# Kernel tuning notes

Hardware: AMD Instinct MI355X
Metric: run time of the kernel (lower is better)

Reference implementation:

```python
import jax, jax.numpy as jnp
import numpy as np

OUTPUT_DIM = 2
HIDDEN_DIM = 512
NUM_MODES = 6
PRED_LEN = 60
BATCH = 8192


def setup_inputs() -> dict:
    key = jax.random.key(0)
    ks = jax.random.split(key, 12)
    H, D, M = HIDDEN_DIM, OUTPUT_DIM, NUM_MODES
    s = 1.0 / np.sqrt(H)  # PyTorch default uniform(-1/sqrt(H), 1/sqrt(H))
    u = lambda k, shape: jax.random.uniform(k, shape, jnp.float32, -s, s)
    return {
        "social_features": jax.random.normal(ks[0], (BATCH, H), jnp.float32),
        "hidden": jax.random.normal(ks[1], (1, BATCH, H), jnp.float32),
        "cell": jax.random.normal(ks[2], (1, BATCH, H), jnp.float32),
        "w_ih": u(ks[3], (4 * H, D + H)),   # LSTM input->gates (i,f,g,o)
        "w_hh": u(ks[4], (4 * H, H)),       # LSTM hidden->gates
        "b_ih": u(ks[5], (4 * H,)),
        "b_hh": u(ks[6], (4 * H,)),
        "w_out": u(ks[7], (D * M, H)),      # output_layer
        "b_out": u(ks[8], (D * M,)),
        "w_mode": u(ks[9], (M, H)),         # mode_prob_layer
        "b_mode": u(ks[10], (M,)),
        "pred_len": PRED_LEN,
    }


def _decode(social_features, hidden, cell, w_ih, w_hh, b_ih, b_hh,
            w_out, b_out, w_mode, b_mode, pred_len):
    B = social_features.shape[0]
    H, D, M = HIDDEN_DIM, OUTPUT_DIM, NUM_MODES
    h0 = hidden[0]  # num_layers == 1
    c0 = cell[0]
    x0 = jnp.zeros((B, D), social_features.dtype)
    bias = b_ih + b_hh

    def step(carry, _):
        x, h, c = carry
        inp = jnp.concatenate([x, social_features], axis=-1)  # [B, D+H]
        gates = inp @ w_ih.T + h @ w_hh.T + bias              # [B, 4H]
        i, f, g, o = jnp.split(gates, 4, axis=-1)             # PyTorch gate order
        i = jax.nn.sigmoid(i)
        f = jax.nn.sigmoid(f)
        g = jnp.tanh(g)
        o = jax.nn.sigmoid(o)
        c_new = f * c + i * g
        h_new = o * jnp.tanh(c_new)
        pred = (h_new @ w_out.T + b_out).reshape(B, M, D)     # [B, M, D]
        mode_prob = jax.nn.softmax(h_new @ w_mode.T + b_mode, axis=-1)  # [B, M]
        x_next = pred[:, 0, :]
        return (x_next, h_new, c_new), (pred, mode_prob)

    _, (preds, probs) = jax.lax.scan(step, (x0, h0, c0), None, length=pred_len)
    # scan stacks on leading time axis -> move to batch-first
    predictions = jnp.transpose(preds, (1, 0, 2, 3))  # [B, T, M, D]
    mode_probs = jnp.transpose(probs, (1, 0, 2))      # [B, T, M]
    return predictions, mode_probs


def reference(social_features, hidden, cell, w_ih, w_hh, b_ih, b_hh,
              w_out, b_out, w_mode, b_mode, pred_len):
    return _decode(social_features, hidden, cell, w_ih, w_hh, b_ih, b_hh,
                   w_out, b_out, w_mode, b_mode, pred_len)
```

## Files before the change

kernel.cpp:

```cpp
#include <hip/hip_runtime.h>

#define H 512
#define BATCHN 8192
#define STEPS 60
#define NWGS 256

#define WEFF_OFF   0u
#define WPLAIN_OFF 2097152u
#define WIHS_OFF   4194304u
#define WSM_OFF    6291456u
#define BSM_OFF    6324224u
#define BX1_OFF    6324352u
#define BX0_OFF    6332544u
#define BAR_OFF    6340736u
#define XCDT_OFF   6340864u
#define FLAGS_OFF  6341888u
#define HB0_OFF    8388608u
#define HB1_OFF    16777216u
#define CPACK_OFF  25165824u
#define SPACK_OFF  41943040u

typedef short s16x8 __attribute__((ext_vector_type(8)));
typedef float f32x4 __attribute__((ext_vector_type(4)));
typedef unsigned int u32x2 __attribute__((ext_vector_type(2)));
typedef unsigned int u32x4 __attribute__((ext_vector_type(4)));

__device__ inline unsigned f2bf(float f) {
  unsigned u = __builtin_bit_cast(unsigned, f);
  return (u + 0x7fffu + ((u >> 16) & 1u)) >> 16;
}
__device__ inline float bf2f(unsigned s) {
  return __builtin_bit_cast(float, s << 16);
}
__device__ inline float sigm(float x) {
  float e = __builtin_amdgcn_exp2f(-1.442695041f * x);
  return __builtin_amdgcn_rcpf(1.0f + e);
}
__device__ inline float tanh_(float x) {
  float e = __builtin_amdgcn_exp2f(2.885390082f * x);
  return 1.0f - 2.0f * __builtin_amdgcn_rcpf(1.0f + e);
}
__device__ inline f32x4 mfma16(s16x8 a, s16x8 b, f32x4 c) {
  return __builtin_amdgcn_mfma_f32_16x16x32_bf16(a, b, c, 0, 0, 0);
}
__device__ inline int haddr(int b, int k) {
  return b * 1024 + ((k * 2) ^ ((b & 7) << 4));
}

__device__ inline void vm_drain() {
  asm volatile("s_waitcnt vmcnt(0)" ::: "memory");
  __builtin_amdgcn_sched_barrier(0);
}

__device__ inline void stage_issue(const unsigned short* h_in, int b0, int p, int tid,
                                   bool fast, u32x4 sreg[4]) {
  const char* pb = (const char*)h_in + (size_t)(b0 + p * 32 + (tid >> 4)) * 1024 +
                   (tid & 15) * 64;
  if (fast) {
    asm volatile("global_load_dwordx4 %0, %1, off sc0" : "=v"(sreg[0]) : "v"(pb));
    asm volatile("global_load_dwordx4 %0, %1, off offset:16 sc0" : "=v"(sreg[1]) : "v"(pb));
    asm volatile("global_load_dwordx4 %0, %1, off offset:32 sc0" : "=v"(sreg[2]) : "v"(pb));
    asm volatile("global_load_dwordx4 %0, %1, off offset:48 sc0" : "=v"(sreg[3]) : "v"(pb));
  } else {
    asm volatile("global_load_dwordx4 %0, %1, off sc0 sc1" : "=v"(sreg[0]) : "v"(pb));
    asm volatile("global_load_dwordx4 %0, %1, off offset:16 sc0 sc1" : "=v"(sreg[1]) : "v"(pb));
    asm volatile("global_load_dwordx4 %0, %1, off offset:32 sc0 sc1" : "=v"(sreg[2]) : "v"(pb));
    asm volatile("global_load_dwordx4 %0, %1, off offset:48 sc0 sc1" : "=v"(sreg[3]) : "v"(pb));
  }
}
__device__ inline void stage_write(unsigned short* buf, int tid, const u32x4 sreg[4]) {
  int row = tid >> 4;
  char* b = (char*)buf + row * 1024;
  int off = (tid & 15) * 64;
  #pragma unroll
  for (int i = 0; i < 4; ++i)
    *(u32x4*)(b + ((off + i * 16) ^ ((row & 7) << 4))) = sreg[i];
}

__device__ inline void global_barrier_once(unsigned* bar) {
  __syncthreads();
  if (threadIdx.x == 0) {
    unsigned a = __hip_atomic_fetch_add(bar, 1u, __ATOMIC_ACQ_REL, __HIP_MEMORY_SCOPE_AGENT);
    if (a == NWGS - 1) {
      __hip_atomic_store(bar + 16, 1u, __ATOMIC_RELEASE, __HIP_MEMORY_SCOPE_AGENT);
    } else {
      #pragma unroll 1
      while (__hip_atomic_load(bar + 16, __ATOMIC_ACQUIRE, __HIP_MEMORY_SCOPE_AGENT) == 0u)
        __builtin_amdgcn_s_sleep(2);
    }
  }
  __syncthreads();
}

__global__ void pack_kernel(const float* __restrict__ w_ih, const float* __restrict__ w_hh,
                            const float* __restrict__ w_out, const float* __restrict__ b_out,
                            const float* __restrict__ w_mode, const float* __restrict__ b_mode,
                            unsigned char* __restrict__ ws) {
  unsigned idx = blockIdx.x * 256 + threadIdx.x;
  if (idx < 2097152u) {
    unsigned j = idx & 1048575u;
    bool eff = idx < 1048576u;
    unsigned e = j & 7u, lane = (j >> 3) & 63u, kb = (j >> 9) & 15u, T = j >> 13;
    unsigned i = lane & 15u;
    unsigned hcol = T * 4u + (i >> 2), gate = i & 3u;
    unsigned n = gate * 512u + hcol;
    unsigned k = kb * 32u + (lane >> 4) * 8u + e;
    float v = w_hh[(size_t)n * 512u + k];
    if (eff) v += w_ih[(size_t)n * 514u] * w_out[k] + w_ih[(size_t)n * 514u + 1u] * w_out[512u + k];
    ((unsigned short*)(ws + (eff ? WEFF_OFF : WPLAIN_OFF)))[j] = (unsigned short)f2bf(v);
  } else if (idx < 3145728u) {
    unsigned j = idx - 2097152u;
    unsigned e = j & 7u, lane = (j >> 3) & 63u, kb = (j >> 9) & 15u, nb = j >> 13;
    unsigned n = nb * 16u + (lane & 15u), k = kb * 32u + (lane >> 4) * 8u + e;
    ((unsigned short*)(ws + WIHS_OFF))[j] = (unsigned short)f2bf(w_ih[(size_t)n * 514u + 2u + k]);
  } else if (idx < 3162112u) {
    unsigned j = idx - 3145728u;
    unsigned e = j & 7u, lane = (j >> 3) & 63u, kb = (j >> 9) & 15u, nb = j >> 13;
    unsigned o = nb * 16u + (lane & 15u), k = kb * 32u + (lane >> 4) * 8u + e;
    float v = 0.0f;
    if (o < 12u) v = w_out[o * 512u + k];
    else if (o < 18u) v = w_mode[(o - 12u) * 512u + k];
    ((unsigned short*)(ws + WSM_OFF))[j] = (unsigned short)f2bf(v);
  } else if (idx < 3162144u) {
    unsigned o = idx - 3162112u;
    float v = 0.0f;
    if (o < 12u) v = b_out[o];
    else if (o < 18u) v = b_mode[o - 12u];
    ((float*)(ws + BSM_OFF))[o] = v;
  } else if (idx < 3164192u) {
    unsigned m = idx - 3162144u;
    unsigned T = m >> 4, i = m & 15u;
    unsigned hcol = T * 4u + (i >> 2), gate = i & 3u;
    unsigned n = gate * 512u + hcol;
    ((float*)(ws + BX1_OFF))[m] = w_ih[(size_t)n * 514u] * b_out[0] + w_ih[(size_t)n * 514u + 1u] * b_out[1];
  } else if (idx < 3166240u) {
    ((float*)(ws + BX0_OFF))[idx - 3164192u] = 0.0f;
  } else if (idx < 3166272u) {
    ((unsigned*)(ws + BAR_OFF))[idx - 3166240u] = 0u;
  } else if (idx < 3166528u) {
    ((unsigned*)(ws + XCDT_OFF))[idx - 3166272u] = 0xFFFFFFFFu;
  } else if (idx < 3168576u) {
    ((unsigned*)(ws + FLAGS_OFF))[idx - 3166528u] = 0u;
  }
}

__global__ __launch_bounds__(512, 2) void prep_kernel(
    const float* __restrict__ social, const float* __restrict__ hidden,
    const float* __restrict__ cell, const float* __restrict__ b_ih,
    const float* __restrict__ b_hh, unsigned char* __restrict__ ws) {
  const int tid = threadIdx.x;
  const int wid = tid >> 6;
  const int lane = tid & 63;
  const int q = lane >> 4;
  const int r = lane & 15;
  const int wg = blockIdx.x;
  const int gb0 = wg * 32;

  const s16x8* wihs_w = (const s16x8*)(ws + WIHS_OFF) + (size_t)wid * 4096 + lane;
  unsigned short* spack = (unsigned short*)(ws + SPACK_OFF);
  unsigned short* hb0 = (unsigned short*)(ws + HB0_OFF);
  float* cpackp = (float*)(ws + CPACK_OFF);

  __shared__ unsigned short h_lds[32 * H];

  s16x8 wbuf[4][4];
  #pragma unroll
  for (int d = 0; d < 4; ++d)
    #pragma unroll
    for (int g = 0; g < 4; ++g)
      wbuf[d][g] = wihs_w[g * 32768 + d * 64];

  #pragma unroll
  for (int i = 0; i < 8; ++i) {
    int rr = i * 4 + (tid >> 7);
    int kk = (tid & 127) * 4;
    f32x4 v = *(const f32x4*)(social + (size_t)(gb0 + rr) * H + kk);
    u32x2 p;
    p[0] = f2bf(v[0]) | (f2bf(v[1]) << 16);
    p[1] = f2bf(v[2]) | (f2bf(v[3]) << 16);
    *(u32x2*)((char*)h_lds + haddr(rr, kk)) = p;
  }
  __syncthreads();

  #pragma unroll
  for (int jb = 0; jb < 4; ++jb) {
    f32x4 acc[4][2];
    #pragma unroll
    for (int g = 0; g < 4; ++g) {
      int n0 = g * 512 + wid * 64 + jb * 16 + q * 4;
      f32x4 bi = *(const f32x4*)(b_ih + n0);
      f32x4 bh = *(const f32x4*)(b_hh + n0);
      f32x4 bias = bi + bh;
      acc[g][0] = bias; acc[g][1] = bias;
    }
    #pragma unroll
    for (int kb = 0; kb < 16; ++kb) {
      const int F = jb * 16 + kb;
      const int slot = F & 3;
      s16x8 bfrag[2];
      #pragma unroll
      for (int bb = 0; bb < 2; ++bb)
        bfrag[bb] = *(const s16x8*)((char*)h_lds + haddr(bb * 16 + r, kb * 32 + q * 8));
      s16x8 af[4];
      #pragma unroll
      for (int g = 0; g < 4; ++g) af[g] = wbuf[slot][g];
      {
        const int Fn = (F + 4) & 63;
        const int jn = Fn >> 4, kn = Fn & 15;
        #pragma unroll
        for (int g = 0; g < 4; ++g)
          wbuf[slot][g] = wihs_w[g * 32768 + jn * 1024 + kn * 64];
      }
      #pragma unroll
      for (int g = 0; g < 4; ++g) {
        acc[g][0] = mfma16(af[g], bfrag[0], acc[g][0]);
        acc[g][1] = mfma16(af[g], bfrag[1], acc[g][1]);
      }
    }
    #pragma unroll
    for (int bb = 0; bb < 2; ++bb) {
      unsigned wrd[8];
      #pragma unroll
      for (int j = 0; j < 8; ++j) {
        int e = j >> 1, gp = (j & 1) * 2;
        wrd[j] = f2bf(acc[gp][bb][e]) | (f2bf(acc[gp + 1][bb][e]) << 16);
      }
      int T = wid * 16 + jb * 4 + q;
      int b = gb0 + bb * 16 + r;
      char* dst = (char*)spack + ((size_t)T * 8192 + b) * 32;
      u32x4 w0; w0[0] = wrd[0]; w0[1] = wrd[1]; w0[2] = wrd[2]; w0[3] = wrd[3];
      u32x4 w1; w1[0] = wrd[4]; w1[1] = wrd[5]; w1[2] = wrd[6]; w1[3] = wrd[7];
      *(u32x4*)dst = w0;
      *(u32x4*)(dst + 16) = w1;
    }
  }

  {
    const float* hsrc = hidden + (size_t)gb0 * H;
    unsigned short* hdst = hb0 + (size_t)gb0 * H;
    int base = tid * 32;
    #pragma unroll
    for (int v8 = 0; v8 < 4; ++v8) {
      f32x4 x0 = *(const f32x4*)(hsrc + base + v8 * 8);
      f32x4 x1 = *(const f32x4*)(hsrc + base + v8 * 8 + 4);
      u32x4 pk;
      pk[0] = f2bf(x0[0]) | (f2bf(x0[1]) << 16);
      pk[1] = f2bf(x0[2]) | (f2bf(x0[3]) << 16);
      pk[2] = f2bf(x1[0]) | (f2bf(x1[1]) << 16);
      pk[3] = f2bf(x1[2]) | (f2bf(x1[3]) << 16);
      *(u32x4*)(hdst + base + v8 * 8) = pk;
    }
  }

  for (int j = 0; j < 32; ++j) {
    int flat = tid * 32 + j;
    int b = gb0 + (flat >> 9);
    int hcol = flat & 511;
    float v = cell[(size_t)b * 512 + hcol];
    int jg2 = hcol >> 6, w2 = (hcol >> 3) & 7, Tl = (hcol >> 2) & 1, q2 = hcol & 3;
    int bg2 = b >> 8, ib2 = (b >> 4) & 15, r2 = b & 15;
    int wg2 = jg2 * 32 + bg2;
    cpackp[(((size_t)(wg2 * 8 + w2) * 16 + ib2) * 2 + Tl) * 64 + q2 * 16 + r2] = v;
  }
}

__global__ __attribute__((amdgpu_flat_work_group_size(512, 512), amdgpu_waves_per_eu(2, 2)))
void coop_kernel(
    const s16x8* __restrict__ weff, const s16x8* __restrict__ wplain,
    const float* __restrict__ bx, const unsigned short* __restrict__ spack,
    const s16x8* __restrict__ wsm, const float* __restrict__ bsm,
    unsigned short* __restrict__ hb0, unsigned short* __restrict__ hb1,
    float* __restrict__ cpack, float* __restrict__ out,
    unsigned* __restrict__ flags, unsigned* __restrict__ xcdt,
    unsigned* __restrict__ bar) {
  const int tid = threadIdx.x;
  const int wid = tid >> 6;
  const int lane = tid & 63;
  const int q = lane >> 4;
  const int r = lane & 15;
  const int wg = blockIdx.x;
  const int jg = wg >> 5;
  const int bg = wg & 31;
  const int b0 = bg * 256;
  const size_t MODE_BASE = (size_t)BATCHN * 720;

  __shared__ s16x8 wsm_lds[2048];
  __shared__ unsigned short hinA[32 * 512];
  __shared__ unsigned short hinB[32 * 512];
  __shared__ unsigned short hout_lds[256 * 64];
  __shared__ float mode_lds[8][16][8];
  __shared__ int fastf_lds;

  unsigned xcd;
  asm volatile("s_getreg_b32 %0, hwreg(20, 0, 32)" : "=s"(xcd));
  if (tid == 0)
    __hip_atomic_store(&xcdt[wg], xcd & 0xFu, __ATOMIC_RELEASE, __HIP_MEMORY_SCOPE_AGENT);

  s16x8 A0[16], A1[16];
  {
    const s16x8* ab = wplain + (size_t)((jg * 16 + wid * 2) * 16) * 64 + lane;
    #pragma unroll
    for (int kb = 0; kb < 16; ++kb) {
      asm volatile("global_load_dwordx4 %0, %1, off" : "=v"(A0[kb]) : "v"(ab + kb * 64));
      asm volatile("global_load_dwordx4 %0, %1, off" : "=v"(A1[kb]) : "v"(ab + kb * 64 + 1024));
    }
  }
  vm_drain();

  float* cb = cpack + (size_t)(wg * 8 + wid) * 2048 + lane;

  #pragma unroll
  for (int i = 0; i < 4; ++i) wsm_lds[i * 512 + tid] = wsm[i * 512 + tid];

  const char* sp0 = (const char*)spack + ((size_t)(jg * 16 + wid * 2 + 0) * 8192) * 32 + q * 8;
  const char* sp1 = (const char*)spack + ((size_t)(jg * 16 + wid * 2 + 1) * 8192) * 32 + q * 8;

  global_barrier_once(bar);
  if (tid == 0) {
    unsigned mine = xcd & 0xFu;
    bool same = true;
    for (int j = 0; j < 8; ++j) {
      unsigned v = __hip_atomic_load(&xcdt[bg + 32 * j], __ATOMIC_ACQUIRE, __HIP_MEMORY_SCOPE_AGENT);
      same = same && (v == mine);
    }
    fastf_lds = same ? 1 : 0;
  }
  __syncthreads();
  const bool fast = (fastf_lds != 0);

  #pragma unroll 1
  for (int s = 0; s < STEPS; ++s) {
    const unsigned short* h_in = (s & 1) ? hb1 : hb0;
    unsigned short* h_out = (s & 1) ? hb0 : hb1;
    f32x4 bxv0 = *(const f32x4*)(bx + (jg * 16 + wid * 2 + 0) * 16 + q * 4);
    f32x4 bxv1 = *(const f32x4*)(bx + (jg * 16 + wid * 2 + 1) * 16 + q * 4);
    if (s == 0) {
      f32x4 z = {0.f, 0.f, 0.f, 0.f};
      bxv0 = z; bxv1 = z;
    }

    u32x4 sreg[4];
    stage_issue(h_in, b0, 0, tid, fast, sreg);
    vm_drain();
    stage_write(hinA, tid, sreg);
    stage_issue(h_in, b0, 1, tid, fast, sreg);
    u32x2 sv0 = *(const u32x2*)(sp0 + (size_t)(b0 + r) * 32);
    u32x2 sv1 = *(const u32x2*)(sp1 + (size_t)(b0 + r) * 32);
    float cvn0 = cb[0], cvn1 = cb[64];
    __syncthreads();

    #pragma unroll
    for (int rr = 0; rr < 8; ++rr) {
      if (rr < 7) {
        unsigned short* wb = ((rr + 1) & 1) ? hinB : hinA;
        vm_drain();
        stage_write(wb, tid, sreg);
        if (rr < 6) stage_issue(h_in, b0, rr + 2, tid, fast, sreg);
      }
      const unsigned short* hbuf = (rr & 1) ? hinB : hinA;
      const bool dop = (wid == rr) && (s > 0);
      #pragma unroll
      for (int ib2 = 0; ib2 < 2; ++ib2) {
        const int bt = rr * 2 + ib2;
        const int b = b0 + bt * 16 + r;
        u32x2 cs0 = sv0, cs1 = sv1;
        float cva0 = cvn0, cva1 = cvn1;
        if (bt < 15) {
          sv0 = *(const u32x2*)(sp0 + (size_t)(b + 16) * 32);
          sv1 = *(const u32x2*)(sp1 + (size_t)(b + 16) * 32);
          cvn0 = cb[(bt + 1) * 128];
          cvn1 = cb[(bt + 1) * 128 + 64];
        }
        f32x4 acc0, acc1;
        acc0[0] = bf2f(cs0[0] & 0xffffu) + bxv0[0];
        acc0[1] = bf2f(cs0[0] >> 16)     + bxv0[1];
        acc0[2] = bf2f(cs0[1] & 0xffffu) + bxv0[2];
        acc0[3] = bf2f(cs0[1] >> 16)     + bxv0[3];
        acc1[0] = bf2f(cs1[0] & 0xffffu) + bxv1[0];
        acc1[1] = bf2f(cs1[0] >> 16)     + bxv1[1];
        acc1[2] = bf2f(cs1[1] & 0xffffu) + bxv1[2];
        acc1[3] = bf2f(cs1[1] >> 16)     + bxv1[3];
        #pragma unroll
        for (int kb = 0; kb < 16; ++kb) {
          s16x8 bfrag = *(const s16x8*)((const char*)hbuf + (ib2 * 16 + r) * 1024 +
                          ((kb * 64 + q * 16) ^ ((r & 7) << 4)));
          acc0 = mfma16(A0[kb], bfrag, acc0);
          acc1 = mfma16(A1[kb], bfrag, acc1);
        }
        #pragma unroll
        for (int Tl = 0; Tl < 2; ++Tl) {
          f32x4 ac = Tl ? acc1 : acc0;
          float cold = Tl ? cva1 : cva0;
          float iv = sigm(ac[0]), fv = sigm(ac[1]), gv = tanh_(ac[2]), ov = sigm(ac[3]);
          float cn = fv * cold + iv * gv;
          cb[bt * 128 + Tl * 64] = cn;
          float hn = ov * tanh_(cn);
          int col = wid * 8 + Tl * 4 + q;
          int row = bt * 16 + r;
          *(unsigned short*)((char*)hout_lds + row * 128 + ((col * 2) ^ ((r & 7) << 4))) =
              (unsigned short)f2bf(hn);
        }
        if (dop) {
          const int tprev = s - 1;
          f32x4 p0 = *(const f32x4*)(bsm + q * 4);
          f32x4 p1 = *(const f32x4*)(bsm + 16 + q * 4);
          #pragma unroll
          for (int kb = 0; kb < 16; ++kb) {
            s16x8 bfrag = *(const s16x8*)((const char*)hbuf + (ib2 * 16 + r) * 1024 +
                            ((kb * 64 + q * 16) ^ ((r & 7) << 4)));
            p0 = mfma16(wsm_lds[kb * 64 + lane], bfrag, p0);
            p1 = mfma16(wsm_lds[(16 + kb) * 64 + lane], bfrag, p1);
          }
          if (q < 3) *(f32x4*)(out + ((size_t)b * 60 + tprev) * 12 + q * 4) = p0;
          if (q == 3) *(f32x4*)(&mode_lds[wid][r][0]) = p0;
          if (q == 0) { mode_lds[wid][r][4] = p1[0]; mode_lds[wid][r][5] = p1[1]; }
          if (q == 1) {
            float v0 = mode_lds[wid][r][0], v1 = mode_lds[wid][r][1], v2 = mode_lds[wid][r][2];
            float v3 = mode_lds[wid][r][3], v4 = mode_lds[wid][r][4], v5 = mode_lds[wid][r][5];
            float mx = fmaxf(fmaxf(fmaxf(v0, v1), fmaxf(v2, v3)), fmaxf(v4, v5));
            float e0 = __builtin_amdgcn_exp2f(1.442695041f * (v0 - mx));
            float e1 = __builtin_amdgcn_exp2f(1.442695041f * (v1 - mx));
            float e2 = __builtin_amdgcn_exp2f(1.442695041f * (v2 - mx));
            float e3 = __builtin_amdgcn_exp2f(1.442695041f * (v3 - mx));
            float e4 = __builtin_amdgcn_exp2f(1.442695041f * (v4 - mx));
            float e5 = __builtin_amdgcn_exp2f(1.442695041f * (v5 - mx));
            float su = e0 + e1 + e2 + e3 + e4 + e5;
            float inv = __builtin_amdgcn_rcpf(su);
            float* mo = out + MODE_BASE + (size_t)b * 360 + tprev * 6;
            mo[0] = e0 * inv; mo[1] = e1 * inv; mo[2] = e2 * inv;
            mo[3] = e3 * inv; mo[4] = e4 * inv; mo[5] = e5 * inv;
          }
        }
      }
      __syncthreads();
    }
    {
      int row = tid >> 1;
      int off0 = (tid & 1) * 64;
      u32x4 v0 = *(const u32x4*)((const char*)hout_lds + row * 128 + ((off0 +  0) ^ ((row & 7) << 4)));
      u32x4 v1 = *(const u32x4*)((const char*)hout_lds + row * 128 + ((off0 + 16) ^ ((row & 7) << 4)));
      u32x4 v2 = *(const u32x4*)((const char*)hout_lds + row * 128 + ((off0 + 32) ^ ((row & 7) << 4)));
      u32x4 v3 = *(const u32x4*)((const char*)hout_lds + row * 128 + ((off0 + 48) ^ ((row & 7) << 4)));
      char* dst = (char*)h_out + (size_t)(b0 + row) * 1024 + jg * 128 + off0;
      if (fast) {
        asm volatile(
            "global_store_dwordx4 %0, %1, off\n\t"
            "global_store_dwordx4 %0, %2, off offset:16\n\t"
            "global_store_dwordx4 %0, %3, off offset:32\n\t"
            "global_store_dwordx4 %0, %4, off offset:48"
            :: "v"(dst), "v"(v0), "v"(v1), "v"(v2), "v"(v3) : "memory");
      } else {
        asm volatile(
            "global_store_dwordx4 %0, %1, off sc0 sc1\n\t"
            "global_store_dwordx4 %0, %2, off offset:16 sc0 sc1\n\t"
            "global_store_dwordx4 %0, %3, off offset:32 sc0 sc1\n\t"
            "global_store_dwordx4 %0, %4, off offset:48 sc0 sc1"
            :: "v"(dst), "v"(v0), "v"(v1), "v"(v2), "v"(v3) : "memory");
      }
      asm volatile("s_waitcnt vmcnt(0)" ::: "memory");
    }
    if (s < STEPS - 1) {
      __syncthreads();
      if (tid == 0) {
        unsigned* f = &flags[bg * 64 + s];
        __hip_atomic_fetch_add(f, 1u, __ATOMIC_RELAXED, __HIP_MEMORY_SCOPE_AGENT);
        unsigned v;
        #pragma unroll 1
        do {
          v = __hip_atomic_load(f, __ATOMIC_RELAXED, __HIP_MEMORY_SCOPE_AGENT);
          if (v < 8u) __builtin_amdgcn_s_sleep(1);
        } while (v < 8u);
      }
      __syncthreads();
    }
    if (s == 0) {
      const s16x8* ab = weff + (size_t)((jg * 16 + wid * 2) * 16) * 64 + lane;
      #pragma unroll
      for (int kb = 0; kb < 16; ++kb) {
        asm volatile("global_load_dwordx4 %0, %1, off" : "=v"(A0[kb]) : "v"(ab + kb * 64));
        asm volatile("global_load_dwordx4 %0, %1, off" : "=v"(A1[kb]) : "v"(ab + kb * 64 + 1024));
      }
      vm_drain();
    }
  }
}

__global__ __launch_bounds__(256) void projf_kernel(
    const unsigned short* __restrict__ h_in, const s16x8* __restrict__ wsm,
    const float* __restrict__ bsm, float* __restrict__ out) {
  const int tid = threadIdx.x;
  const int wid = tid >> 6;
  const int lane = tid & 63;
  const int q = lane >> 4;
  const int r = lane & 15;
  const int wg = blockIdx.x;
  const int b0 = wg * 32;
  const int bt = wid & 1, T = wid >> 1;
  const size_t MODE_BASE = (size_t)BATCHN * 720;
  __shared__ float mbuf[32][8];

  u32x4 hf[16];
  const char* hbase = (const char*)h_in + (size_t)(b0 + bt * 16 + r) * 1024 + q * 16;
  #pragma unroll
  for (int g = 0; g < 16; ++g) {
    asm volatile("global_load_dwordx4 %0, %1, off sc0 sc1"
                 : "=v"(hf[g]) : "v"(hbase + g * 64));
  }
  asm volatile("s_waitcnt vmcnt(0)" ::: "memory");
  __builtin_amdgcn_sched_barrier(0);

  f32x4 pacc = *(const f32x4*)(bsm + T * 16 + q * 4);
  #pragma unroll
  for (int kb = 0; kb < 16; ++kb) {
    s16x8 bfrag = __builtin_bit_cast(s16x8, hf[kb]);
    s16x8 af = wsm[(T * 16 + kb) * 64 + lane];
    pacc = mfma16(af, bfrag, pacc);
  }
  int b = b0 + bt * 16 + r;
  if (T == 0) {
    if (q < 3) *(f32x4*)(out + ((size_t)b * 60 + 59) * 12 + q * 4) = pacc;
    if (q == 3) *(f32x4*)(&mbuf[bt * 16 + r][0]) = pacc;
  } else {
    if (q == 0) { mbuf[bt * 16 + r][4] = pacc[0]; mbuf[bt * 16 + r][5] = pacc[1]; }
  }
  __syncthreads();
  if (tid < 32) {
    float v0 = mbuf[tid][0], v1 = mbuf[tid][1], v2 = mbuf[tid][2];
    float v3 = mbuf[tid][3], v4 = mbuf[tid][4], v5 = mbuf[tid][5];
    float mx = fmaxf(fmaxf(fmaxf(v0, v1), fmaxf(v2, v3)), fmaxf(v4, v5));
    float e0 = __builtin_amdgcn_exp2f(1.442695041f * (v0 - mx));
    float e1 = __builtin_amdgcn_exp2f(1.442695041f * (v1 - mx));
    float e2 = __builtin_amdgcn_exp2f(1.442695041f * (v2 - mx));
    float e3 = __builtin_amdgcn_exp2f(1.442695041f * (v3 - mx));
    float e4 = __builtin_amdgcn_exp2f(1.442695041f * (v4 - mx));
    float e5 = __builtin_amdgcn_exp2f(1.442695041f * (v5 - mx));
    float s = e0 + e1 + e2 + e3 + e4 + e5;
    float inv = __builtin_amdgcn_rcpf(s);
    float* mo = out + MODE_BASE + (size_t)(b0 + tid) * 360 + 59 * 6;
    mo[0] = e0 * inv; mo[1] = e1 * inv; mo[2] = e2 * inv;
    mo[3] = e3 * inv; mo[4] = e4 * inv; mo[5] = e5 * inv;
  }
}

extern "C" void kernel_launch(void* const* d_in, const int* in_sizes, int n_in,
                              void* d_out, int out_size, void* d_ws, size_t ws_size,
                              hipStream_t stream) {
  const float* social = (const float*)d_in[0];
  const float* hidden = (const float*)d_in[1];
  const float* cell   = (const float*)d_in[2];
  const float* w_ih   = (const float*)d_in[3];
  const float* w_hh   = (const float*)d_in[4];
  const float* b_ih   = (const float*)d_in[5];
  const float* b_hh   = (const float*)d_in[6];
  const float* w_out  = (const float*)d_in[7];
  const float* b_out  = (const float*)d_in[8];
  const float* w_mode = (const float*)d_in[9];
  const float* b_mode = (const float*)d_in[10];
  unsigned char* ws = (unsigned char*)d_ws;
  float* out = (float*)d_out;

  hipLaunchKernelGGL(pack_kernel, dim3((3168576u + 255u) / 256u), dim3(256), 0, stream,
                     w_ih, w_hh, w_out, b_out, w_mode, b_mode, ws);
  hipLaunchKernelGGL(prep_kernel, dim3(256), dim3(512), 0, stream,
                     social, hidden, cell, b_ih, b_hh, ws);

  const s16x8* weff   = (const s16x8*)(ws + WEFF_OFF);
  const s16x8* wplain = (const s16x8*)(ws + WPLAIN_OFF);
  const s16x8* wsm    = (const s16x8*)(ws + WSM_OFF);
  const float* bsm    = (const float*)(ws + BSM_OFF);
  const float* bx1    = (const float*)(ws + BX1_OFF);
  const unsigned short* spack = (const unsigned short*)(ws + SPACK_OFF);
  unsigned short* hb0p = (unsigned short*)(ws + HB0_OFF);
  unsigned short* hb1p = (unsigned short*)(ws + HB1_OFF);
  float* cpackc = (float*)(ws + CPACK_OFF);
  unsigned* flagsp = (unsigned*)(ws + FLAGS_OFF);
  unsigned* xcdtp = (unsigned*)(ws + XCDT_OFF);
  unsigned* barp = (unsigned*)(ws + BAR_OFF);

  void* args[] = {(void*)&weff, (void*)&wplain, (void*)&bx1, (void*)&spack,
                  (void*)&wsm, (void*)&bsm, (void*)&hb0p, (void*)&hb1p,
                  (void*)&cpackc, (void*)&out, (void*)&flagsp, (void*)&xcdtp,
                  (void*)&barp};
  hipLaunchCooperativeKernel((const void*)coop_kernel, dim3(NWGS), dim3(512),
                             args, 0, stream);

  hipLaunchKernelGGL(projf_kernel, dim3(256), dim3(256), 0, stream,
                     hb0p, wsm, bsm, out);
}
```

Measured before the change: 4.103 ms.

## Restructure per-round load pipeline with counted vmcnt waits and LDS-cached biases

Reworks the inner round loop of the persistent LSTM kernel so the h-tile staging write and the next-next issue happen after the MFMA compute instead of before it. Cell-state and social-precompute loads for a whole round are issued ahead through inline asm. Full vmcnt(0) drains become partial waits so loads overlap compute. Bias vectors (bx, bsm) are cached in LDS, and stores go through inline asm so they do not disturb the vmcnt accounting. Correctness depends on the hand-counted vmcnt values matching the actual order of outstanding loads and stores.

```diff
diff --git a/kernel.cpp b/kernel.cpp
--- a/kernel.cpp
+++ b/kernel.cpp
@@ -46,28 +46,14 @@
 __device__ inline int haddr(int b, int k) {
   return b * 1024 + ((k * 2) ^ ((b & 7) << 4));
 }
-
 __device__ inline void vm_drain() {
   asm volatile("s_waitcnt vmcnt(0)" ::: "memory");
   __builtin_amdgcn_sched_barrier(0);
 }
-
-__device__ inline void stage_issue(const unsigned short* h_in, int b0, int p, int tid,
-                                   bool fast, u32x4 sreg[4]) {
-  const char* pb = (const char*)h_in + (size_t)(b0 + p * 32 + (tid >> 4)) * 1024 +
-                   (tid & 15) * 64;
-  if (fast) {
-    asm volatile("global_load_dwordx4 %0, %1, off sc0" : "=v"(sreg[0]) : "v"(pb));
-    asm volatile("global_load_dwordx4 %0, %1, off offset:16 sc0" : "=v"(sreg[1]) : "v"(pb));
-    asm volatile("global_load_dwordx4 %0, %1, off offset:32 sc0" : "=v"(sreg[2]) : "v"(pb));
-    asm volatile("global_load_dwordx4 %0, %1, off offset:48 sc0" : "=v"(sreg[3]) : "v"(pb));
-  } else {
-    asm volatile("global_load_dwordx4 %0, %1, off sc0 sc1" : "=v"(sreg[0]) : "v"(pb));
-    asm volatile("global_load_dwordx4 %0, %1, off offset:16 sc0 sc1" : "=v"(sreg[1]) : "v"(pb));
-    asm volatile("global_load_dwordx4 %0, %1, off offset:32 sc0 sc1" : "=v"(sreg[2]) : "v"(pb));
-    asm volatile("global_load_dwordx4 %0, %1, off offset:48 sc0 sc1" : "=v"(sreg[3]) : "v"(pb));
-  }
-}
+#define WAITV(n) do { \
+  asm volatile("s_waitcnt vmcnt(" #n ")" ::: "memory"); \
+  __builtin_amdgcn_sched_barrier(0); } while (0)
+
 __device__ inline void stage_write(unsigned short* buf, int tid, const u32x4 sreg[4]) {
   int row = tid >> 4;
   char* b = (char*)buf + row * 1024;
@@ -289,6 +275,8 @@
   __shared__ unsigned short hinB[32 * 512];
   __shared__ unsigned short hout_lds[256 * 64];
   __shared__ float mode_lds[8][16][8];
+  __shared__ float bx_lds[256];
+  __shared__ float bsm_lds[32];
   __shared__ int fastf_lds;
 
   unsigned xcd;
@@ -308,12 +296,13 @@
   vm_drain();
 
   float* cb = cpack + (size_t)(wg * 8 + wid) * 2048 + lane;
+  const char* sp0b = (const char*)spack + ((size_t)(jg * 16 + wid * 2 + 0) * 8192 + (b0 + r)) * 32 + q * 8;
+  const char* sp1b = (const char*)spack + ((size_t)(jg * 16 + wid * 2 + 1) * 8192 + (b0 + r)) * 32 + q * 8;
 
   #pragma unroll
   for (int i = 0; i < 4; ++i) wsm_lds[i * 512 + tid] = wsm[i * 512 + tid];
-
-  const char* sp0 = (const char*)spack + ((size_t)(jg * 16 + wid * 2 + 0) * 8192) * 32 + q * 8;
-  const char* sp1 = (const char*)spack + ((size_t)(jg * 16 + wid * 2 + 1) * 8192) * 32 + q * 8;
+  if (tid < 256) bx_lds[tid] = bx[jg * 256 + tid];
+  if (tid < 32) bsm_lds[tid] = bsm[tid];
 
   global_barrier_once(bar);
   if (tid == 0) {
@@ -328,58 +317,82 @@
   __syncthreads();
   const bool fast = (fastf_lds != 0);
 
+  u32x4 sreg[4];
+  u32x2 sv_e0, sv_e1, sv_o0, sv_o1;
+  float cv_e0, cv_e1, cv_o0, cv_o1;
+
+#define ISSUE_H(p) do { \
+    const char* pb_ = (const char*)h_in + (size_t)(b0 + (p) * 32 + (tid >> 4)) * 1024 + (tid & 15) * 64; \
+    if (fast) { \
+      asm volatile("global_load_dwordx4 %0, %1, off sc0" : "=v"(sreg[0]) : "v"(pb_)); \
+      asm volatile("global_load_dwordx4 %0, %1, off offset:16 sc0" : "=v"(sreg[1]) : "v"(pb_)); \
+      asm volatile("global_load_dwordx4 %0, %1, off offset:32 sc0" : "=v"(sreg[2]) : "v"(pb_)); \
+      asm volatile("global_load_dwordx4 %0, %1, off offset:48 sc0" : "=v"(sreg[3]) : "v"(pb_)); \
+    } else { \
+      asm volatile("global_load_dwordx4 %0, %1, off sc0 sc1" : "=v"(sreg[0]) : "v"(pb_)); \
+      asm volatile("global_load_dwordx4 %0, %1, off offset:16 sc0 sc1" : "=v"(sreg[1]) : "v"(pb_)); \
+      asm volatile("global_load_dwordx4 %0, %1, off offset:32 sc0 sc1" : "=v"(sreg[2]) : "v"(pb_)); \
+      asm volatile("global_load_dwordx4 %0, %1, off offset:48 sc0 sc1" : "=v"(sreg[3]) : "v"(pb_)); \
+    } } while (0)
+
+#define ISSUE_SC(p) do { \
+    asm volatile("global_load_dwordx2 %0, %1, off" : "=v"(sv_e0) : "v"(sp0b + (p) * 1024)); \
+    asm volatile("global_load_dwordx2 %0, %1, off" : "=v"(sv_e1) : "v"(sp1b + (p) * 1024)); \
+    asm volatile("global_load_dwordx2 %0, %1, off" : "=v"(sv_o0) : "v"(sp0b + (p) * 1024 + 512)); \
+    asm volatile("global_load_dwordx2 %0, %1, off" : "=v"(sv_o1) : "v"(sp1b + (p) * 1024 + 512)); \
+    asm volatile("global_load_dword %0, %1, off" : "=v"(cv_e0) : "v"(cb + (p) * 256)); \
+    asm volatile("global_load_dword %0, %1, off" : "=v"(cv_e1) : "v"(cb + (p) * 256 + 64)); \
+    asm volatile("global_load_dword %0, %1, off" : "=v"(cv_o0) : "v"(cb + (p) * 256 + 128)); \
+    asm volatile("global_load_dword %0, %1, off" : "=v"(cv_o1) : "v"(cb + (p) * 256 + 192)); \
+  } while (0)
+
   #pragma unroll 1
   for (int s = 0; s < STEPS; ++s) {
     const unsigned short* h_in = (s & 1) ? hb1 : hb0;
     unsigned short* h_out = (s & 1) ? hb0 : hb1;
-    f32x4 bxv0 = *(const f32x4*)(bx + (jg * 16 + wid * 2 + 0) * 16 + q * 4);
-    f32x4 bxv1 = *(const f32x4*)(bx + (jg * 16 + wid * 2 + 1) * 16 + q * 4);
+    f32x4 bz0 = *(const f32x4*)&bx_lds[wid * 32 + q * 4];
+    f32x4 bz1 = *(const f32x4*)&bx_lds[wid * 32 + 16 + q * 4];
     if (s == 0) {
       f32x4 z = {0.f, 0.f, 0.f, 0.f};
-      bxv0 = z; bxv1 = z;
-    }
-
-    u32x4 sreg[4];
-    stage_issue(h_in, b0, 0, tid, fast, sreg);
-    vm_drain();
+      bz0 = z; bz1 = z;
+    }
+
+    ISSUE_H(0);
+    ISSUE_SC(0);
+    WAITV(0);
     stage_write(hinA, tid, sreg);
-    stage_issue(h_in, b0, 1, tid, fast, sreg);
-    u32x2 sv0 = *(const u32x2*)(sp0 + (size_t)(b0 + r) * 32);
-    u32x2 sv1 = *(const u32x2*)(sp1 + (size_t)(b0 + r) * 32);
-    float cvn0 = cb[0], cvn1 = cb[64];
+    ISSUE_H(1);
     __syncthreads();
 
     #pragma unroll
     for (int rr = 0; rr < 8; ++rr) {
-      if (rr < 7) {
-        unsigned short* wb = ((rr + 1) & 1) ? hinB : hinA;
-        vm_drain();
-        stage_write(wb, tid, sreg);
-        if (rr < 6) stage_issue(h_in, b0, rr + 2, tid, fast, sreg);
-      }
-      const unsigned short* hbuf = (rr & 1) ? hinB : hinA;
+      const int k = rr & 1;
+      if (rr == 7)      WAITV(0);
+      else if (rr > 0)  WAITV(4);
+
+      u32x2 ps_e0 = sv_e0, ps_e1 = sv_e1, ps_o0 = sv_o0, ps_o1 = sv_o1;
+      float pc_e0 = cv_e0, pc_e1 = cv_e1, pc_o0 = cv_o0, pc_o1 = cv_o1;
+      if (rr < 7) ISSUE_SC(rr + 1);
+
+      const unsigned short* hbuf = k ? hinB : hinA;
       const bool dop = (wid == rr) && (s > 0);
       #pragma unroll
       for (int ib2 = 0; ib2 < 2; ++ib2) {
         const int bt = rr * 2 + ib2;
         const int b = b0 + bt * 16 + r;
-        u32x2 cs0 = sv0, cs1 = sv1;
-        float cva0 = cvn0, cva1 = cvn1;
-        if (bt < 15) {
-          sv0 = *(const u32x2*)(sp0 + (size_t)(b + 16) * 32);
-          sv1 = *(const u32x2*)(sp1 + (size_t)(b + 16) * 32);
-          cvn0 = cb[(bt + 1) * 128];
-          cvn1 = cb[(bt + 1) * 128 + 64];
-        }
+        u32x2 cs0 = ib2 ? ps_o0 : ps_e0;
+        u32x2 cs1 = ib2 ? ps_o1 : ps_e1;
+        float cva0 = ib2 ? pc_o0 : pc_e0;
+        float cva1 = ib2 ? pc_o1 : pc_e1;
         f32x4 acc0, acc1;
-        acc0[0] = bf2f(cs0[0] & 0xffffu) + bxv0[0];
-        acc0[1] = bf2f(cs0[0] >> 16)     + bxv0[1];
-        acc0[2] = bf2f(cs0[1] & 0xffffu) + bxv0[2];
-        acc0[3] = bf2f(cs0[1] >> 16)     + bxv0[3];
-        acc1[0] = bf2f(cs1[0] & 0xffffu) + bxv1[0];
-        acc1[1] = bf2f(cs1[0] >> 16)     + bxv1[1];
-        acc1[2] = bf2f(cs1[1] & 0xffffu) + bxv1[2];
-        acc1[3] = bf2f(cs1[1] >> 16)     + bxv1[3];
+        acc0[0] = bf2f(cs0[0] & 0xffffu) + bz0[0];
+        acc0[1] = bf2f(cs0[0] >> 16)     + bz0[1];
+        acc0[2] = bf2f(cs0[1] & 0xffffu) + bz0[2];
+        acc0[3] = bf2f(cs0[1] >> 16)     + bz0[3];
+        acc1[0] = bf2f(cs1[0] & 0xffffu) + bz1[0];
+        acc1[1] = bf2f(cs1[0] >> 16)     + bz1[1];
+        acc1[2] = bf2f(cs1[1] & 0xffffu) + bz1[2];
+        acc1[3] = bf2f(cs1[1] >> 16)     + bz1[3];
         #pragma unroll
         for (int kb = 0; kb < 16; ++kb) {
           s16x8 bfrag = *(const s16x8*)((const char*)hbuf + (ib2 * 16 + r) * 1024 +
@@ -393,7 +406,8 @@
           float cold = Tl ? cva1 : cva0;
           float iv = sigm(ac[0]), fv = sigm(ac[1]), gv = tanh_(ac[2]), ov = sigm(ac[3]);
           float cn = fv * cold + iv * gv;
-          cb[bt * 128 + Tl * 64] = cn;
+          asm volatile("global_store_dword %0, %1, off"
+                       :: "v"(cb + bt * 128 + Tl * 64), "v"(cn));
           float hn = ov * tanh_(cn);
           int col = wid * 8 + Tl * 4 + q;
           int row = bt * 16 + r;
@@ -402,8 +416,8 @@
         }
         if (dop) {
           const int tprev = s - 1;
-          f32x4 p0 = *(const f32x4*)(bsm + q * 4);
-          f32x4 p1 = *(const f32x4*)(bsm + 16 + q * 4);
+          f32x4 p0 = *(const f32x4*)&bsm_lds[q * 4];
+          f32x4 p1 = *(const f32x4*)&bsm_lds[16 + q * 4];
           #pragma unroll
           for (int kb = 0; kb < 16; ++kb) {
             s16x8 bfrag = *(const s16x8*)((const char*)hbuf + (ib2 * 16 + r) * 1024 +
@@ -411,7 +425,9 @@
             p0 = mfma16(wsm_lds[kb * 64 + lane], bfrag, p0);
             p1 = mfma16(wsm_lds[(16 + kb) * 64 + lane], bfrag, p1);
           }
-          if (q < 3) *(f32x4*)(out + ((size_t)b * 60 + tprev) * 12 + q * 4) = p0;
+          if (q < 3)
+            asm volatile("global_store_dwordx4 %0, %1, off"
+                         :: "v"(out + ((size_t)b * 60 + tprev) * 12 + q * 4), "v"(p0));
           if (q == 3) *(f32x4*)(&mode_lds[wid][r][0]) = p0;
           if (q == 0) { mode_lds[wid][r][4] = p1[0]; mode_lds[wid][r][5] = p1[1]; }
           if (q == 1) {
@@ -427,13 +443,27 @@
             float su = e0 + e1 + e2 + e3 + e4 + e5;
             float inv = __builtin_amdgcn_rcpf(su);
             float* mo = out + MODE_BASE + (size_t)b * 360 + tprev * 6;
-            mo[0] = e0 * inv; mo[1] = e1 * inv; mo[2] = e2 * inv;
-            mo[3] = e3 * inv; mo[4] = e4 * inv; mo[5] = e5 * inv;
+            u32x2 m01, m23, m45;
+            m01[0] = __builtin_bit_cast(unsigned, e0 * inv);
+            m01[1] = __builtin_bit_cast(unsigned, e1 * inv);
+            m23[0] = __builtin_bit_cast(unsigned, e2 * inv);
+            m23[1] = __builtin_bit_cast(unsigned, e3 * inv);
+            m45[0] = __builtin_bit_cast(unsigned, e4 * inv);
+            m45[1] = __builtin_bit_cast(unsigned, e5 * inv);
+            asm volatile("global_store_dwordx2 %0, %1, off" :: "v"(mo), "v"(m01));
+            asm volatile("global_store_dwordx2 %0, %1, off" :: "v"(mo + 2), "v"(m23));
+            asm volatile("global_store_dwordx2 %0, %1, off" :: "v"(mo + 4), "v"(m45));
           }
         }
       }
+      if (rr < 7) {
+        WAITV(8);
+        stage_write(((rr + 1) & 1) ? hinB : hinA, tid, sreg);
+        if (rr <= 5) ISSUE_H(rr + 2);
+      }
       __syncthreads();
     }
+
     {
       int row = tid >> 1;
       int off0 = (tid & 1) * 64;
@@ -483,6 +513,8 @@
       vm_drain();
     }
   }
+#undef ISSUE_H
+#undef ISSUE_SC
 }
 
 __global__ __launch_bounds__(256) void projf_kernel(
```

After: 4.561 ms. 1.11x slower.
